# Kernel optimization log

Measured on AMD Instinct MI355X. Metric: run time of the kernel, lower is better.

The kernel has to match this reference:

```python
import jax, jax.numpy as jnp
import numpy as np

B, S = 256, 32
XSIZE, YSIZE = 64, 64
LABEL_SIZE = 24
DEFAULT_LABEL = 0


def setup_inputs() -> dict:
    key = jax.random.key(0)
    ks = jax.random.split(key, 12)
    inp = {
        'pred_left': jax.random.normal(ks[0], (B, S, XSIZE), jnp.float32),
        'pred_top': jax.random.normal(ks[1], (B, S, YSIZE), jnp.float32),
        'pred_width': jax.random.normal(ks[2], (B, S, XSIZE), jnp.float32),
        'pred_height': jax.random.normal(ks[3], (B, S, YSIZE), jnp.float32),
        'pred_label': jax.random.normal(ks[4], (B, S, LABEL_SIZE), jnp.float32),
        'true_left': jax.random.randint(ks[5], (B, S), 0, XSIZE, jnp.int32),
        'true_top': jax.random.randint(ks[6], (B, S), 0, YSIZE, jnp.int32),
        'true_width': jax.random.randint(ks[7], (B, S), 0, 32, jnp.int32),
        'true_height': jax.random.randint(ks[8], (B, S), 0, 32, jnp.int32),
        'true_label': jax.random.randint(ks[9], (B, S), 0, LABEL_SIZE, jnp.int32),
        'true_length': jax.random.randint(ks[10], (B,), 0, S + 1, jnp.int32),
        'pred_length': jax.random.randint(ks[11], (B,), 0, S + 1, jnp.int32),
    }
    return inp


def _make_gridmaps(left, top, width, height, label, mask):
    right = jnp.minimum(XSIZE - 1, left + width)    # [B,S]
    bottom = jnp.minimum(YSIZE - 1, top + height)   # [B,S]
    # original skips boxes with top>=bottom or left>=right
    valid = mask & (top < bottom) & (left < right)
    ys = jnp.arange(YSIZE, dtype=jnp.int32)
    xs = jnp.arange(XSIZE, dtype=jnp.int32)
    cov_y = (top[:, :, None] <= ys) & (ys <= bottom[:, :, None])   # [B,S,Y]
    cov_x = (left[:, :, None] <= xs) & (xs <= right[:, :, None])   # [B,S,X]
    cover = valid[:, :, None, None] & cov_y[:, :, :, None] & cov_x[:, :, None, :]  # [B,S,Y,X]
    j = jnp.arange(S, dtype=jnp.int32)
    last = jnp.max(jnp.where(cover, j[None, :, None, None], -1), axis=1)  # [B,Y,X]
    gathered = jnp.take_along_axis(
        label, jnp.clip(last, 0, S - 1).reshape(label.shape[0], -1), axis=1
    ).reshape(last.shape)
    return jnp.where(last >= 0, gathered, DEFAULT_LABEL)


def _compute_acc_miou(map_true, map_pred):
    b = map_true.shape[0]
    bidx = jnp.arange(b, dtype=jnp.int32)[:, None]
    pred = map_pred.reshape(b, -1)
    true = map_true.reshape(b, -1)
    confusion = jnp.zeros((b, LABEL_SIZE, LABEL_SIZE), jnp.int32).at[bidx, pred, true].add(1)
    confusion = confusion.astype(jnp.float32)
    inter = jnp.diagonal(confusion, axis1=1, axis2=2)
    union = confusion.sum(axis=1) + confusion.sum(axis=2) - inter
    acc = inter.sum(axis=1) / confusion.sum(axis=(1, 2))
    weight = (union > 0).astype(jnp.float32)
    iou = inter / (union + 1e-9)
    miou = (weight * iou).sum(axis=1) / weight.sum(axis=1)
    return acc, miou


def reference(pred_left, pred_top, pred_width, pred_height, pred_label,
              true_left, true_top, true_width, true_height, true_label,
              true_length, pred_length):
    seq = jnp.arange(S, dtype=jnp.int32)
    mask_true = seq[None, :] < true_length[:, None]
    mask_pred = seq[None, :] < pred_length[:, None]
    map_true = _make_gridmaps(true_left, true_top, true_width, true_height,
                              true_label, mask_true)
    # from_logits: argmax over last dim (stop_gradient in original)
    pl = jnp.argmax(jax.lax.stop_gradient(pred_left), axis=-1).astype(jnp.int32)
    pt = jnp.argmax(jax.lax.stop_gradient(pred_top), axis=-1).astype(jnp.int32)
    pw = jnp.argmax(jax.lax.stop_gradient(pred_width), axis=-1).astype(jnp.int32)
    ph = jnp.argmax(jax.lax.stop_gradient(pred_height), axis=-1).astype(jnp.int32)
    plab = jnp.argmax(jax.lax.stop_gradient(pred_label), axis=-1).astype(jnp.int32)
    map_pred = _make_gridmaps(pl, pt, pw, ph, plab, mask_pred)
    acc, miou = _compute_acc_miou(map_true, map_pred)
    return acc, miou
```

## Files before the change

### kernel.cpp

```cpp
#include <hip/hip_runtime.h>

#define NB 256
#define S  32
#define NL 24

__global__ __launch_bounds__(512) void layout_metric_kernel(
    const float* __restrict__ pred_left,
    const float* __restrict__ pred_top,
    const float* __restrict__ pred_width,
    const float* __restrict__ pred_height,
    const float* __restrict__ pred_label,
    const int* __restrict__ true_left,
    const int* __restrict__ true_top,
    const int* __restrict__ true_width,
    const int* __restrict__ true_height,
    const int* __restrict__ true_label,
    const int* __restrict__ true_length,
    const int* __restrict__ pred_length,
    float* __restrict__ out)
{
    const int b   = blockIdx.x;
    const int tid = threadIdx.x;

    __shared__ int s_arg[5][S];
    __shared__ unsigned long long s_xmask[2][S];
    __shared__ unsigned int s_meta[2][S];
    __shared__ unsigned long long s_M[2][64][NL];
    __shared__ int s_cnt[3][NL];

    if (tid < 256) {
        const int type = tid >> 6;
        const int j    = (tid >> 1) & 31;
        const int half = tid & 1;
        const float* base = (type == 0) ? pred_left
                          : (type == 1) ? pred_top
                          : (type == 2) ? pred_width
                                        : pred_height;
        const float4* r4 = (const float4*)(base + ((size_t)b * S + j) * 64) + half * 8;
        float best = -3.402823466e38f;
        int   bi   = half * 32;
        #pragma unroll
        for (int k = 0; k < 8; ++k) {
            float4 v = r4[k];
            const int o = half * 32 + 4 * k;
            if (v.x > best) { best = v.x; bi = o + 0; }
            if (v.y > best) { best = v.y; bi = o + 1; }
            if (v.z > best) { best = v.z; bi = o + 2; }
            if (v.w > best) { best = v.w; bi = o + 3; }
        }
        const float ob = __shfl_xor(best, 1);
        const int   oi = __shfl_xor(bi, 1);
        if (half == 0) {
            if (ob > best) { bi = oi; }
            s_arg[type][j] = bi;
        }
    } else if (tid < 288) {
        const int j = tid - 256;
        const float4* r4 = (const float4*)(pred_label + ((size_t)b * S + j) * NL);
        float best = -3.402823466e38f;
        int   bi   = 0;
        #pragma unroll
        for (int k = 0; k < 6; ++k) {
            float4 v = r4[k];
            if (v.x > best) { best = v.x; bi = 4 * k + 0; }
            if (v.y > best) { best = v.y; bi = 4 * k + 1; }
            if (v.z > best) { best = v.z; bi = 4 * k + 2; }
            if (v.w > best) { best = v.w; bi = 4 * k + 3; }
        }
        s_arg[4][j] = bi;
    } else if (tid >= 320 && tid < 352) {
        const int j   = tid - 320;
        const int l   = true_left  [b * S + j];
        const int t   = true_top   [b * S + j];
        const int w   = true_width [b * S + j];
        const int h   = true_height[b * S + j];
        const int lab = true_label [b * S + j];
        const int len = true_length[b];
        const int r  = min(63, l + w);
        const int bo = min(63, t + h);
        const bool val = (j < len) && (t < bo) && (l < r);
        unsigned long long xm = 0ull;
        if (val) xm = (~0ull << l) & (~0ull >> (63 - r));
        s_xmask[0][j] = xm;
        s_meta[0][j]  = (val ? 0x80000000u : 0u) |
                        ((unsigned)t << 12) | ((unsigned)bo << 6) | (unsigned)lab;
    } else if (tid >= 352 && tid < 352 + 3 * NL) {
        (&s_cnt[0][0])[tid - 352] = 0;
    }

    {
        unsigned long long* mflat = &s_M[0][0][0];
        #pragma unroll
        for (int k = 0; k < 6; ++k) mflat[tid + k * 512] = 0ull;
    }
    __syncthreads();

    if (tid < S) {
        const int j   = tid;
        const int l   = s_arg[0][j];
        const int t   = s_arg[1][j];
        const int w   = s_arg[2][j];
        const int h   = s_arg[3][j];
        const int lab = s_arg[4][j];
        const int len = pred_length[b];
        const int r  = min(63, l + w);
        const int bo = min(63, t + h);
        const bool val = (j < len) && (t < bo) && (l < r);
        unsigned long long xm = 0ull;
        if (val) xm = (~0ull << l) & (~0ull >> (63 - r));
        s_xmask[1][j] = xm;
        s_meta[1][j]  = (val ? 0x80000000u : 0u) |
                        ((unsigned)t << 12) | ((unsigned)bo << 6) | (unsigned)lab;
    }
    __syncthreads();

    if (tid < 128) {
        const int m = tid >> 6;
        const int y = tid & 63;
        unsigned long long rem = ~0ull;
        #pragma unroll
        for (int j = S - 1; j >= 0; --j) {
            const unsigned int md = s_meta[m][j];
            if (md & 0x80000000u) {
                const int top = (md >> 12) & 63;
                const int bot = (md >> 6)  & 63;
                if (top <= y && y <= bot) {
                    const unsigned long long cov = s_xmask[m][j] & rem;
                    if (cov) {
                        rem &= ~cov;
                        s_M[m][y][md & 31] |= cov;
                    }
                }
            }
        }
        if (rem) s_M[m][y][0] |= rem;
    }
    __syncthreads();

    if (tid < 8 * NL) {
        const int L  = tid % NL;
        const int rg = tid / NL;
        int ct = 0, cp = 0, ci = 0;
        #pragma unroll
        for (int i = 0; i < 8; ++i) {
            const int y = rg * 8 + i;
            const unsigned long long tm = s_M[0][y][L];
            const unsigned long long pm = s_M[1][y][L];
            ct += __popcll(tm);
            cp += __popcll(pm);
            ci += __popcll(tm & pm);
        }
        atomicAdd(&s_cnt[0][L], ct);
        atomicAdd(&s_cnt[1][L], cp);
        atomicAdd(&s_cnt[2][L], ci);
    }
    __syncthreads();

    if (tid < 64) {
        float it_p = 0.f, ws_p = 0.f, wi_p = 0.f;
        if (tid < NL) {
            const int ct = s_cnt[0][tid];
            const int cp = s_cnt[1][tid];
            const int ci = s_cnt[2][tid];
            const int un = ct + cp - ci;
            it_p = (float)ci;
            if (un > 0) {
                ws_p = 1.f;
                wi_p = (float)ci / ((float)un + 1e-9f);
            }
        }
        #pragma unroll
        for (int m = 32; m >= 1; m >>= 1) {
            it_p += __shfl_xor(it_p, m);
            ws_p += __shfl_xor(ws_p, m);
            wi_p += __shfl_xor(wi_p, m);
        }
        if (tid == 0) {
            out[b]      = it_p / 4096.0f;
            out[NB + b] = wi_p / ws_p;
        }
    }
}

extern "C" void kernel_launch(void* const* d_in, const int* in_sizes, int n_in,
                              void* d_out, int out_size, void* d_ws, size_t ws_size,
                              hipStream_t stream) {
    const float* pred_left   = (const float*)d_in[0];
    const float* pred_top    = (const float*)d_in[1];
    const float* pred_width  = (const float*)d_in[2];
    const float* pred_height = (const float*)d_in[3];
    const float* pred_label  = (const float*)d_in[4];
    const int*   true_left   = (const int*)d_in[5];
    const int*   true_top    = (const int*)d_in[6];
    const int*   true_width  = (const int*)d_in[7];
    const int*   true_height = (const int*)d_in[8];
    const int*   true_label  = (const int*)d_in[9];
    const int*   true_length = (const int*)d_in[10];
    const int*   pred_length = (const int*)d_in[11];
    float* out = (float*)d_out;

    layout_metric_kernel<<<NB, 512, 0, stream>>>(
        pred_left, pred_top, pred_width, pred_height, pred_label,
        true_left, true_top, true_width, true_height, true_label,
        true_length, pred_length, out);
}
```

Measured before the change: 13.07 us.

## Rasterize labels into bit-planes and write transposed label masks without zero-init

Per-row rasterization now keeps five 64-bit bit-planes that encode each pixel's label. It then decodes all 24 label masks and writes them directly into a transposed s_M[m][L][y] layout, so the shared-memory zero-fill and the scattered OR updates are no longer needed. The popcount stage reads contiguous 128-bit shared loads per label and reduces with wave shuffles instead of shared atomics. The argmax loops keep four independent running maxima and merge them at the end, which shortens the dependency chain. The cost is that every row thread always writes 24 masks, and the argmax tie-breaking has to match first-index semantics.

```diff
diff --git a/kernel.cpp b/kernel.cpp
--- a/kernel.cpp
+++ b/kernel.cpp
@@ -3,6 +3,9 @@
 #define NB 256
 #define S  32
 #define NL 24
+
+#define COMBINE(va, ia, vb, ib) \
+    do { if ((vb) > (va) || ((vb) == (va) && (ib) < (ia))) { (va) = (vb); (ia) = (ib); } } while (0)
 
 __global__ __launch_bounds__(512) void layout_metric_kernel(
     const float* __restrict__ pred_left,
@@ -25,7 +28,7 @@
     __shared__ int s_arg[5][S];
     __shared__ unsigned long long s_xmask[2][S];
     __shared__ unsigned int s_meta[2][S];
-    __shared__ unsigned long long s_M[2][64][NL];
+    __shared__ unsigned long long s_M[2][NL][64];
     __shared__ int s_cnt[3][NL];
 
     if (tid < 256) {
@@ -37,37 +40,48 @@
                           : (type == 2) ? pred_width
                                         : pred_height;
         const float4* r4 = (const float4*)(base + ((size_t)b * S + j) * 64) + half * 8;
-        float best = -3.402823466e38f;
-        int   bi   = half * 32;
-        #pragma unroll
-        for (int k = 0; k < 8; ++k) {
-            float4 v = r4[k];
+        float4 bv = r4[0];
+        int ix = half * 32 + 0, iy = half * 32 + 1, iz = half * 32 + 2, iw = half * 32 + 3;
+        #pragma unroll
+        for (int k = 1; k < 8; ++k) {
+            const float4 v = r4[k];
             const int o = half * 32 + 4 * k;
-            if (v.x > best) { best = v.x; bi = o + 0; }
-            if (v.y > best) { best = v.y; bi = o + 1; }
-            if (v.z > best) { best = v.z; bi = o + 2; }
-            if (v.w > best) { best = v.w; bi = o + 3; }
-        }
-        const float ob = __shfl_xor(best, 1);
-        const int   oi = __shfl_xor(bi, 1);
+            if (v.x > bv.x) { bv.x = v.x; ix = o + 0; }
+            if (v.y > bv.y) { bv.y = v.y; iy = o + 1; }
+            if (v.z > bv.z) { bv.z = v.z; iz = o + 2; }
+            if (v.w > bv.w) { bv.w = v.w; iw = o + 3; }
+        }
+        float v0 = bv.x; int i0 = ix;
+        COMBINE(v0, i0, bv.y, iy);
+        float v1 = bv.z; int i1 = iz;
+        COMBINE(v1, i1, bv.w, iw);
+        COMBINE(v0, i0, v1, i1);
+        const float ob = __shfl_xor(v0, 1);
+        const int   oi = __shfl_xor(i0, 1);
         if (half == 0) {
-            if (ob > best) { bi = oi; }
-            s_arg[type][j] = bi;
+            if (ob > v0) i0 = oi;
+            s_arg[type][j] = i0;
         }
     } else if (tid < 288) {
         const int j = tid - 256;
         const float4* r4 = (const float4*)(pred_label + ((size_t)b * S + j) * NL);
-        float best = -3.402823466e38f;
-        int   bi   = 0;
-        #pragma unroll
-        for (int k = 0; k < 6; ++k) {
-            float4 v = r4[k];
-            if (v.x > best) { best = v.x; bi = 4 * k + 0; }
-            if (v.y > best) { best = v.y; bi = 4 * k + 1; }
-            if (v.z > best) { best = v.z; bi = 4 * k + 2; }
-            if (v.w > best) { best = v.w; bi = 4 * k + 3; }
-        }
-        s_arg[4][j] = bi;
+        float4 bv = r4[0];
+        int ix = 0, iy = 1, iz = 2, iw = 3;
+        #pragma unroll
+        for (int k = 1; k < 6; ++k) {
+            const float4 v = r4[k];
+            const int o = 4 * k;
+            if (v.x > bv.x) { bv.x = v.x; ix = o + 0; }
+            if (v.y > bv.y) { bv.y = v.y; iy = o + 1; }
+            if (v.z > bv.z) { bv.z = v.z; iz = o + 2; }
+            if (v.w > bv.w) { bv.w = v.w; iw = o + 3; }
+        }
+        float v0 = bv.x; int i0 = ix;
+        COMBINE(v0, i0, bv.y, iy);
+        float v1 = bv.z; int i1 = iz;
+        COMBINE(v1, i1, bv.w, iw);
+        COMBINE(v0, i0, v1, i1);
+        s_arg[4][j] = i0;
     } else if (tid >= 320 && tid < 352) {
         const int j   = tid - 320;
         const int l   = true_left  [b * S + j];
@@ -84,14 +98,6 @@
         s_xmask[0][j] = xm;
         s_meta[0][j]  = (val ? 0x80000000u : 0u) |
                         ((unsigned)t << 12) | ((unsigned)bo << 6) | (unsigned)lab;
-    } else if (tid >= 352 && tid < 352 + 3 * NL) {
-        (&s_cnt[0][0])[tid - 352] = 0;
-    }
-
-    {
-        unsigned long long* mflat = &s_M[0][0][0];
-        #pragma unroll
-        for (int k = 0; k < 6; ++k) mflat[tid + k * 512] = 0ull;
     }
     __syncthreads();
 
@@ -118,41 +124,58 @@
         const int m = tid >> 6;
         const int y = tid & 63;
         unsigned long long rem = ~0ull;
+        unsigned long long pl0 = 0, pl1 = 0, pl2 = 0, pl3 = 0, pl4 = 0;
         #pragma unroll
         for (int j = S - 1; j >= 0; --j) {
             const unsigned int md = s_meta[m][j];
             if (md & 0x80000000u) {
                 const int top = (md >> 12) & 63;
                 const int bot = (md >> 6)  & 63;
-                if (top <= y && y <= bot) {
-                    const unsigned long long cov = s_xmask[m][j] & rem;
-                    if (cov) {
-                        rem &= ~cov;
-                        s_M[m][y][md & 31] |= cov;
-                    }
-                }
+                const unsigned long long cov =
+                    (top <= y && y <= bot) ? (s_xmask[m][j] & rem) : 0ull;
+                rem &= ~cov;
+                const unsigned lab = md & 31;
+                if (lab & 1u)  pl0 |= cov;
+                if (lab & 2u)  pl1 |= cov;
+                if (lab & 4u)  pl2 |= cov;
+                if (lab & 8u)  pl3 |= cov;
+                if (lab & 16u) pl4 |= cov;
             }
         }
-        if (rem) s_M[m][y][0] |= rem;
+        const unsigned long long n0 = ~pl0, n1 = ~pl1, n2 = ~pl2, n3 = ~pl3, n4 = ~pl4;
+        #pragma unroll
+        for (int L = 0; L < NL; ++L) {
+            const unsigned long long mk = ((L & 1)  ? pl0 : n0)
+                                        & ((L & 2)  ? pl1 : n1)
+                                        & ((L & 4)  ? pl2 : n2)
+                                        & ((L & 8)  ? pl3 : n3)
+                                        & ((L & 16) ? pl4 : n4);
+            s_M[m][L][y] = mk;
+        }
     }
     __syncthreads();
 
     if (tid < 8 * NL) {
-        const int L  = tid % NL;
-        const int rg = tid / NL;
+        const int L  = tid >> 3;
+        const int rg = tid & 7;
+        const ulonglong2* pt = (const ulonglong2*)&s_M[0][L][rg * 8];
+        const ulonglong2* pp = (const ulonglong2*)&s_M[1][L][rg * 8];
         int ct = 0, cp = 0, ci = 0;
         #pragma unroll
-        for (int i = 0; i < 8; ++i) {
-            const int y = rg * 8 + i;
-            const unsigned long long tm = s_M[0][y][L];
-            const unsigned long long pm = s_M[1][y][L];
-            ct += __popcll(tm);
-            cp += __popcll(pm);
-            ci += __popcll(tm & pm);
-        }
-        atomicAdd(&s_cnt[0][L], ct);
-        atomicAdd(&s_cnt[1][L], cp);
-        atomicAdd(&s_cnt[2][L], ci);
+        for (int i = 0; i < 4; ++i) {
+            const ulonglong2 a = pt[i];
+            const ulonglong2 c = pp[i];
+            ct += __popcll(a.x) + __popcll(a.y);
+            cp += __popcll(c.x) + __popcll(c.y);
+            ci += __popcll(a.x & c.x) + __popcll(a.y & c.y);
+        }
+        #pragma unroll
+        for (int d = 1; d < 8; d <<= 1) {
+            ct += __shfl_xor(ct, d);
+            cp += __shfl_xor(cp, d);
+            ci += __shfl_xor(ci, d);
+        }
+        if (rg == 0) { s_cnt[0][L] = ct; s_cnt[1][L] = cp; s_cnt[2][L] = ci; }
     }
     __syncthreads();
 
```

Measured after the change: 14.66 us, median of 2. 1.12x slower.
